# Optimization experiments

Hardware: AMD Instinct MI355X
Metric: run time of the kernel (lower is better)

Reference implementation:

```python
import jax, jax.numpy as jnp
import numpy as np

B, N, D, H, P, S = 2, 40962, 128, 4, 100, 512
HD = D // H  # 32
EPS = 1e-5


def setup_inputs() -> dict:
    key = jax.random.key(0)
    ks = jax.random.split(key, 8)
    s = 1.0 / np.sqrt(D)
    x = jax.random.normal(ks[0], (B, N, D), jnp.float32)
    Wq = jax.random.normal(ks[1], (D, D), jnp.float32) * s
    Wk = jax.random.normal(ks[2], (D, D), jnp.float32) * s
    Wv = jax.random.normal(ks[3], (D, D), jnp.float32) * s
    Wo = jax.random.normal(ks[4], (D, D), jnp.float32) * s
    bq = jnp.zeros((D,), jnp.float32)
    bk = jnp.zeros((D,), jnp.float32)
    bv = jnp.zeros((D,), jnp.float32)
    bo = jnp.zeros((D,), jnp.float32)
    ln_g = jnp.ones((D,), jnp.float32)
    ln_b = jnp.zeros((D,), jnp.float32)
    patch_indices = jax.random.randint(ks[5], (P, S), 0, N)  # node ids per patch slot
    core_mask = jax.random.uniform(ks[6], (P, S)) < 0.8       # core vs overlap slots
    return dict(x=x, Wq=Wq, bq=bq, Wk=Wk, bk=bk, Wv=Wv, bv=bv, Wo=Wo, bo=bo,
                ln_g=ln_g, ln_b=ln_b, patch_indices=patch_indices, core_mask=core_mask)


def reference(x, Wq, bq, Wk, bk, Wv, bv, Wo, bo, ln_g, ln_b, patch_indices, core_mask):
    # gather: [B, P, S, D]
    px = x[:, patch_indices]

    def proj(W, b):
        return (px @ W.T + b).reshape(B, P, S, H, HD)

    q = proj(Wq, bq)
    k = proj(Wk, bk)
    v = proj(Wv, bv)

    # per-patch multi-head attention
    scores = jnp.einsum('bpshd,bpthd->bphst', q, k) / np.sqrt(HD).astype(np.float32)
    attn = jax.nn.softmax(scores, axis=-1)  # dropout is identity in eval
    att = jnp.einsum('bphst,bpthd->bpshd', attn, v).reshape(B, P, S, D)
    patch_out = att @ Wo.T + bo  # [B, P, S, D]

    # scatter-add only core slots back to nodes, with overlap-count normalization
    cm = core_mask.astype(x.dtype)
    patch_out = patch_out * cm[None, :, :, None]
    idx = patch_indices.reshape(-1)  # [P*S]
    vals = patch_out.reshape(B, P * S, D).transpose(1, 0, 2)  # [P*S, B, D]
    agg = jax.ops.segment_sum(vals, idx, num_segments=N).transpose(1, 0, 2)  # [B, N, D]
    cnt = jax.ops.segment_sum(cm.reshape(-1), idx, num_segments=N)  # [N]
    out = agg / jnp.clip(cnt, 1.0)[None, :, None]

    # residual + LayerNorm
    h = x + out
    mu = jnp.mean(h, axis=-1, keepdims=True)
    var = jnp.mean((h - mu) ** 2, axis=-1, keepdims=True)
    return (h - mu) / jnp.sqrt(var + EPS) * ln_g + ln_b
```

## Files before the change

kernel.cpp:

```cpp
#include <hip/hip_runtime.h>
#include <hip/hip_bf16.h>
#include <hip/hip_fp16.h>

#define B_ 2
#define N_ 40962
#define D_ 128
#define H_ 4
#define P_ 100
#define S_ 512
#define T_ 102400
#define PS_ 51200
#define CAP_ 32

typedef unsigned short u16;
typedef unsigned int u32;
typedef _Float16 f16x4 __attribute__((ext_vector_type(4)));
typedef _Float16 f16x8 __attribute__((ext_vector_type(8)));
typedef float f32x4 __attribute__((ext_vector_type(4)));

#define OFF_Q    0ull
#define OFF_K    26214400ull
#define OFF_V    52428800ull
#define OFF_BP   78643200ull
#define OFF_CNT  78774272ull
#define OFF_CM   78938120ull
#define OFF_FLAG 79142920ull
#define CUR_BYTES ((size_t)N_ * 4)

__device__ __forceinline__ u32 pack2h(float a, float b) {
  __half2 h = __floats2half2_rn(a, b);
  return __builtin_bit_cast(u32, h);
}
__device__ __forceinline__ f16x8 cat8(uint2 lo, uint2 hi) {
  return __builtin_bit_cast(f16x8, make_uint4(lo.x, lo.y, hi.x, hi.y));
}

__device__ __forceinline__ f32x4 mfma32(f16x8 a, f16x8 b, f32x4 c) {
#if __has_builtin(__builtin_amdgcn_mfma_f32_16x16x32_f16)
  return __builtin_amdgcn_mfma_f32_16x16x32_f16(a, b, c, 0, 0, 0);
#else
  f16x4 alo = {a[0], a[1], a[2], a[3]}, ahi = {a[4], a[5], a[6], a[7]};
  f16x4 blo = {b[0], b[1], b[2], b[3]}, bhi = {b[4], b[5], b[6], b[7]};
  c = __builtin_amdgcn_mfma_f32_16x16x16f16(alo, blo, c, 0, 0, 0);
  return __builtin_amdgcn_mfma_f32_16x16x16f16(ahi, bhi, c, 0, 0, 0);
#endif
}

__device__ __forceinline__ bool mask_on(const void* mask, int fl, int i) {
  if (fl & 1) return ((const unsigned char*)mask)[i] != 0;
  if (fl & 2) return ((const float*)mask)[i] != 0.f;
  return ((const int*)mask)[i] != 0;
}

__global__ void probe_mask_k(const unsigned char* __restrict__ mb, int* __restrict__ flag) {
  int i = blockIdx.x * 256 + threadIdx.x;
  int f = 0;
  unsigned char v = mb[i];
  if (v) {
    int m4 = i & 3;
    if (m4 == 1) f |= 1;
    else if (m4 == 3) f |= 2;
  }
#pragma unroll
  for (int m = 32; m >= 1; m >>= 1) f |= __shfl_xor(f, m);
  if ((threadIdx.x & 63) == 0 && f) atomicOr(flag, f);
}

__global__ void mask_cnt_k(const void* __restrict__ mask, const int* __restrict__ pidx,
                           const int* __restrict__ flag, float* __restrict__ cm,
                           float* __restrict__ cnt) {
  int i = blockIdx.x * 256 + threadIdx.x;
  int fl = *flag;
  bool on = mask_on(mask, fl, i);
  cm[i] = on ? 1.f : 0.f;
  if (on) atomicAdd(&cnt[pidx[i]], 1.f);
}

__global__ void fill_k(const void* __restrict__ mask, const int* __restrict__ pidx,
                       const int* __restrict__ flag, int* __restrict__ cursor,
                       int* __restrict__ slots) {
  int i = blockIdx.x * 256 + threadIdx.x;
  int fl = *flag;
  if (mask_on(mask, fl, i)) {
    int n = pidx[i];
    int pos = atomicAdd(&cursor[n], 1);
    if (pos < CAP_) slots[n * CAP_ + pos] = i;
  }
}

__global__ void pack_w_k(const float* __restrict__ Wq, const float* __restrict__ Wk,
                         const float* __restrict__ Wv, const float* __restrict__ Wo,
                         u16* __restrict__ bp) {
  int gi = blockIdx.x * 256 + threadIdx.x;
  int m = gi >> 12;
  int r = gi & 4095;
  int fi = r >> 6;
  int l = r & 63;
  int nt = fi >> 3, ks = fi & 7;
  const float* W = (m == 0) ? Wq : (m == 1) ? Wk : (m == 2) ? Wv : Wo;
  int n = nt * 16 + (l & 15);
  int k0 = ks * 16 + ((l >> 4) << 2);
  float4 w = *(const float4*)(W + n * 128 + k0);
  *(uint2*)(bp + (size_t)gi * 4) = make_uint2(pack2h(w.x, w.y), pack2h(w.z, w.w));
}

__global__ __launch_bounds__(256) void qkv_k(
    const float* __restrict__ x, const int* __restrict__ pidx,
    const u16* __restrict__ bp,
    const float* __restrict__ bq, const float* __restrict__ bk, const float* __restrict__ bv,
    u16* __restrict__ qkv) {
  int tid = threadIdx.x;
  int t0 = blockIdx.x * 64;
  int lane = tid & 63, wid = tid >> 6;
  int l15 = lane & 15, l4 = lane >> 4;
  int wm = wid & 1, wn = wid >> 1;
  uint2 afr[2][8];
#pragma unroll
  for (int tt = 0; tt < 2; tt++) {
    int tok = t0 + wm * 32 + tt * 16 + l15;
    int b = (tok >= PS_) ? 1 : 0;
    int ps = tok - b * PS_;
    int pi = pidx[ps];
    const float* rp = x + ((size_t)b * N_ + pi) * D_;
#pragma unroll
    for (int ks = 0; ks < 8; ks++) {
      float4 f = *(const float4*)(rp + ks * 16 + l4 * 4);
      afr[tt][ks] = make_uint2(
          __builtin_bit_cast(u32, __builtin_amdgcn_cvt_pkrtz(f.x, f.y)),
          __builtin_bit_cast(u32, __builtin_amdgcn_cvt_pkrtz(f.z, f.w)));
    }
  }
  const uint2* bpp = (const uint2*)bp;
  u16* qout = qkv;
  u16* kh = qkv + (size_t)T_ * D_;
  u16* vt = qkv + (size_t)2 * T_ * D_;
#pragma unroll 1
  for (int mat = 0; mat < 3; mat++) {
    uint2 bfrag[4][8];
#pragma unroll
    for (int nt = 0; nt < 4; nt++) {
      int ntg = wn * 4 + nt;
#pragma unroll
      for (int ks = 0; ks < 8; ks++)
        bfrag[nt][ks] = bpp[(mat * 64 + ntg * 8 + ks) * 64 + lane];
    }
    if (mat < 2) {
      const float* bias = (mat == 0) ? bq : bk;
      f32x4 acc[4][2];
#pragma unroll
      for (int nt = 0; nt < 4; nt++) {
        float4 b4 = *(const float4*)(bias + wn * 64 + nt * 16 + l4 * 4);
        f32x4 bz = {b4.x, b4.y, b4.z, b4.w};
        acc[nt][0] = bz;
        acc[nt][1] = bz;
      }
#pragma unroll
      for (int kp = 0; kp < 4; kp++) {
#pragma unroll
        for (int nt = 0; nt < 4; nt++) {
          f16x8 a = cat8(bfrag[nt][2 * kp], bfrag[nt][2 * kp + 1]);
#pragma unroll
          for (int tt = 0; tt < 2; tt++) {
            f16x8 b = cat8(afr[tt][2 * kp], afr[tt][2 * kp + 1]);
            acc[nt][tt] = mfma32(a, b, acc[nt][tt]);
          }
        }
      }
#pragma unroll
      for (int tt = 0; tt < 2; tt++) {
        int tok = t0 + wm * 32 + tt * 16 + l15;
#pragma unroll
        for (int nt = 0; nt < 4; nt++) {
          int n0 = wn * 64 + nt * 16 + l4 * 4;
          f32x4 a = acc[nt][tt];
          uint2 pv = make_uint2(pack2h(a[0], a[1]), pack2h(a[2], a[3]));
          if (mat == 0) {
            *(uint2*)(qout + (size_t)tok * D_ + n0) = pv;
          } else {
            int bpi = tok >> 9, s = tok & 511;
            int ch = n0 >> 5, hd = n0 & 31;
            *(uint2*)(kh + ((size_t)(bpi * 4 + ch) * 512 + s) * 32 + hd) = pv;
          }
        }
      }
    } else {
      f32x4 acc[2][4];
#pragma unroll
      for (int nt = 0; nt < 4; nt++) {
        float bvv = bv[wn * 64 + nt * 16 + l15];
#pragma unroll
        for (int mt = 0; mt < 2; mt++) {
          f32x4 z = {bvv, bvv, bvv, bvv};
          acc[mt][nt] = z;
        }
      }
#pragma unroll
      for (int kp = 0; kp < 4; kp++) {
#pragma unroll
        for (int mt = 0; mt < 2; mt++) {
          f16x8 a = cat8(afr[mt][2 * kp], afr[mt][2 * kp + 1]);
#pragma unroll
          for (int nt = 0; nt < 4; nt++) {
            f16x8 b = cat8(bfrag[nt][2 * kp], bfrag[nt][2 * kp + 1]);
            acc[mt][nt] = mfma32(a, b, acc[mt][nt]);
          }
        }
      }
#pragma unroll
      for (int mt = 0; mt < 2; mt++) {
        int rbase = t0 + wm * 32 + mt * 16 + (l4 << 2);
        int bpi = rbase >> 9;
        int s0 = rbase & 511;
#pragma unroll
        for (int nt = 0; nt < 4; nt++) {
          int col = wn * 64 + nt * 16 + l15;
          uint2 pv = make_uint2(pack2h(acc[mt][nt][0], acc[mt][nt][1]),
                                pack2h(acc[mt][nt][2], acc[mt][nt][3]));
          *(uint2*)(vt + ((size_t)(bpi * 4 + (col >> 5)) * 32 + (col & 31)) * 512 + s0) = pv;
        }
      }
    }
  }
}

__global__ __launch_bounds__(512, 4) void attn_k(
    u16* wq_att, const u16* __restrict__ wk, const u16* __restrict__ wvt) {
  __shared__ __align__(16) u16 Ks[512 * 32];
  __shared__ __align__(16) u16 Vs[32 * 512];
  int tid = threadIdx.x;
  int bid = blockIdx.x;
  int h = bid & 3;
  int bp = bid >> 2;
  int lane = tid & 63, w = tid >> 6;
  int l15 = lane & 15, l4 = lane >> 4;
  size_t tbase = (size_t)bp * 512;
  int q0 = w * 64;
  {
    const u16* kg = wk + (size_t)(bp * 4 + h) * 512 * 32;
    const u16* vg = wvt + (size_t)(bp * 4 + h) * 32 * 512;
#pragma unroll
    for (int j = 0; j < 4; j++) {
      int i = j * 512 + tid;
      uint4 ku = *(const uint4*)(kg + (size_t)i * 8);
      int row = i >> 2, c = i & 3;
      int swk = (row >> 1) & 7;
      *(uint2*)(Ks + row * 32 + (((2 * c)     ^ swk) << 2)) = make_uint2(ku.x, ku.y);
      *(uint2*)(Ks + row * 32 + (((2 * c + 1) ^ swk) << 2)) = make_uint2(ku.z, ku.w);
      uint4 vu = *(const uint4*)(vg + (size_t)i * 8);
      int vr2 = i >> 6, vc = i & 63;
      int swv = vr2 & 15;
      *(uint2*)(Vs + vr2 * 512 + (((2 * vc)     ^ swv) << 2)) = make_uint2(vu.x, vu.y);
      *(uint2*)(Vs + vr2 * 512 + (((2 * vc + 1) ^ swv) << 2)) = make_uint2(vu.z, vu.w);
    }
  }
  uint4 qf8[4];
  {
    const u16* qbase = wq_att + (tbase + q0) * 128 + h * 32;
    const __half2 sc2 = __floats2half2_rn(0.25500527f, 0.25500527f);
#pragma unroll
    for (int nt = 0; nt < 4; nt++) {
      const u16* qr = qbase + (size_t)(nt * 16 + l15) * 128 + l4 * 4;
      uint2 u0 = *(const uint2*)(qr);
      uint2 u1 = *(const uint2*)(qr + 16);
      u32 w0 = __builtin_bit_cast(u32, __hmul2(__builtin_bit_cast(__half2, u0.x), sc2));
      u32 w1 = __builtin_bit_cast(u32, __hmul2(__builtin_bit_cast(__half2, u0.y), sc2));
      u32 w2 = __builtin_bit_cast(u32, __hmul2(__builtin_bit_cast(__half2, u1.x), sc2));
      u32 w3 = __builtin_bit_cast(u32, __hmul2(__builtin_bit_cast(__half2, u1.y), sc2));
      qf8[nt] = make_uint4(w0, w1, w2, w3);
    }
  }
  f32x4 O[2][4];
  f32x4 LS[4];
#pragma unroll
  for (int a = 0; a < 4; a++) {
    O[0][a] = (f32x4){0.f, 0.f, 0.f, 0.f};
    O[1][a] = (f32x4){0.f, 0.f, 0.f, 0.f};
    LS[a] = (f32x4){0.f, 0.f, 0.f, 0.f};
  }
  const f16x8 ones8 = {(_Float16)1.f, (_Float16)1.f, (_Float16)1.f, (_Float16)1.f,
                       (_Float16)1.f, (_Float16)1.f, (_Float16)1.f, (_Float16)1.f};
  __syncthreads();

  for (int t0 = 0; t0 < 512; t0 += 64) {
#pragma unroll
    for (int mp = 0; mp < 2; mp++) {
      int krA = t0 + mp * 32 + l15;
      int krB = krA + 16;
      const u16* kpA = Ks + krA * 32;
      const u16* kpB = Ks + krB * 32;
      int swkA = (krA >> 1) & 7;
      int swkB = (krB >> 1) & 7;
      uint2 a0A = *(const uint2*)(kpA + ((l4       ^ swkA) << 2));
      uint2 a1A = *(const uint2*)(kpA + (((4 + l4) ^ swkA) << 2));
      uint2 a0B = *(const uint2*)(kpB + ((l4       ^ swkB) << 2));
      uint2 a1B = *(const uint2*)(kpB + (((4 + l4) ^ swkB) << 2));
      f16x8 a8A = cat8(a0A, a1A);
      f16x8 a8B = cat8(a0B, a1B);
      int gA = (t0 >> 2) + mp * 8 + l4;
      int gB = gA + 4;
      uint2 vA0 = *(const uint2*)(Vs + l15 * 512        + ((gA ^ l15) << 2));
      uint2 vB0 = *(const uint2*)(Vs + l15 * 512        + ((gB ^ l15) << 2));
      uint2 vA1 = *(const uint2*)(Vs + (16 + l15) * 512 + ((gA ^ l15) << 2));
      uint2 vB1 = *(const uint2*)(Vs + (16 + l15) * 512 + ((gB ^ l15) << 2));
      f16x8 v80 = cat8(vA0, vB0);
      f16x8 v81 = cat8(vA1, vB1);
      __builtin_amdgcn_s_setprio(1);
#pragma unroll
      for (int nt = 0; nt < 4; nt++) {
        f16x8 qb = __builtin_bit_cast(f16x8, qf8[nt]);
        f32x4 z = {0.f, 0.f, 0.f, 0.f};
        f32x4 sA = mfma32(a8A, qb, z);
        f32x4 sB = mfma32(a8B, qb, z);
        float e0 = __builtin_amdgcn_exp2f(sA[0]);
        float e1 = __builtin_amdgcn_exp2f(sA[1]);
        float e2 = __builtin_amdgcn_exp2f(sA[2]);
        float e3 = __builtin_amdgcn_exp2f(sA[3]);
        float e4 = __builtin_amdgcn_exp2f(sB[0]);
        float e5 = __builtin_amdgcn_exp2f(sB[1]);
        float e6 = __builtin_amdgcn_exp2f(sB[2]);
        float e7 = __builtin_amdgcn_exp2f(sB[3]);
        uint4 pu = make_uint4(
            __builtin_bit_cast(u32, __builtin_amdgcn_cvt_pkrtz(e0, e1)),
            __builtin_bit_cast(u32, __builtin_amdgcn_cvt_pkrtz(e2, e3)),
            __builtin_bit_cast(u32, __builtin_amdgcn_cvt_pkrtz(e4, e5)),
            __builtin_bit_cast(u32, __builtin_amdgcn_cvt_pkrtz(e6, e7)));
        f16x8 pb = __builtin_bit_cast(f16x8, pu);
        LS[nt]   = mfma32(ones8, pb, LS[nt]);
        O[0][nt] = mfma32(v80, pb, O[0][nt]);
        O[1][nt] = mfma32(v81, pb, O[1][nt]);
      }
      __builtin_amdgcn_s_setprio(0);
    }
  }
#pragma unroll
  for (int nt = 0; nt < 4; nt++) {
    float r = 1.f / LS[nt][0];
#pragma unroll
    for (int mt2 = 0; mt2 < 2; mt2++) {
      uint2 ov = make_uint2(pack2h(O[mt2][nt][0] * r, O[mt2][nt][1] * r),
                            pack2h(O[mt2][nt][2] * r, O[mt2][nt][3] * r));
      *(uint2*)(wq_att + (tbase + q0 + nt * 16 + l15) * 128 + h * 32 + mt2 * 16 + l4 * 4) = ov;
    }
  }
}

__global__ __launch_bounds__(256) void proj_k(
    const u16* __restrict__ watt, const u16* __restrict__ bp, const float* __restrict__ bo,
    u16* __restrict__ po) {
  __shared__ uint4 As[64 * 16];
  int tid = threadIdx.x;
  int t0 = blockIdx.x * 64;
  {
    int r = tid >> 2, qd = tid & 3;
    const uint4* src = (const uint4*)(watt + (size_t)(t0 + r) * D_ + qd * 32);
#pragma unroll
    for (int c = 0; c < 4; c++) {
      int byteoff = (qd * 64 + c * 16) ^ ((r & 7) << 4);
      As[r * 16 + (byteoff >> 4)] = src[c];
    }
  }
  __syncthreads();
  int lane = tid & 63, wid = tid >> 6;
  int l15 = lane & 15, l4 = lane >> 4;
  int wm = wid & 1, wn = wid >> 1;
  uint2 bfrag[4][8];
  const uint2* bpp = (const uint2*)bp;
#pragma unroll
  for (int nt = 0; nt < 4; nt++) {
    int ntg = wn * 4 + nt;
#pragma unroll
    for (int ks = 0; ks < 8; ks++)
      bfrag[nt][ks] = bpp[(3 * 64 + ntg * 8 + ks) * 64 + lane];
  }
  uint2 afr[2][8];
#pragma unroll
  for (int tt = 0; tt < 2; tt++) {
    int row = wm * 32 + tt * 16 + l15;
#pragma unroll
    for (int ks = 0; ks < 8; ks++) {
      int byteoff = (ks * 32 + (l4 << 3)) ^ ((row & 7) << 4);
      afr[tt][ks] = *(const uint2*)((const char*)As + row * 256 + byteoff);
    }
  }
  f32x4 acc[4][2];
#pragma unroll
  for (int nt = 0; nt < 4; nt++) {
    float4 bo4 = *(const float4*)(bo + wn * 64 + nt * 16 + l4 * 4);
    f32x4 bz = {bo4.x, bo4.y, bo4.z, bo4.w};
    acc[nt][0] = bz;
    acc[nt][1] = bz;
  }
#pragma unroll
  for (int kp = 0; kp < 4; kp++) {
#pragma unroll
    for (int nt = 0; nt < 4; nt++) {
      f16x8 a = cat8(bfrag[nt][2 * kp], bfrag[nt][2 * kp + 1]);
#pragma unroll
      for (int tt = 0; tt < 2; tt++) {
        f16x8 b = cat8(afr[tt][2 * kp], afr[tt][2 * kp + 1]);
        acc[nt][tt] = mfma32(a, b, acc[nt][tt]);
      }
    }
  }
#pragma unroll
  for (int tt = 0; tt < 2; tt++) {
    size_t tok = t0 + wm * 32 + tt * 16 + l15;
#pragma unroll
    for (int nt = 0; nt < 4; nt++) {
      int n0 = wn * 64 + nt * 16 + l4 * 4;
      f32x4 a = acc[nt][tt];
      uint2 pv = make_uint2(pack2h(a[0], a[1]), pack2h(a[2], a[3]));
      *(uint2*)(po + tok * D_ + n0) = pv;
    }
  }
}

__global__ __launch_bounds__(256) void ln_k(
    const float* __restrict__ x, const float* __restrict__ cnt,
    const u16* __restrict__ po, const int* __restrict__ slots,
    const float* __restrict__ g, const float* __restrict__ bta, float* __restrict__ out) {
  int tid = threadIdx.x;
  int row = blockIdx.x * 8 + (tid >> 5);
  if (row >= B_ * N_) return;
  int l32 = tid & 31;
  int n = row % N_;
  int b = row / N_;
  float c = cnt[n];
  int deg = (int)c;
  if (deg > CAP_) deg = CAP_;
  float rc = 1.f / (c > 1.f ? c : 1.f);
  float4 a = make_float4(0.f, 0.f, 0.f, 0.f);
  const int* sl = slots + n * CAP_;
  for (int j = 0; j < deg; j++) {
    int s = sl[j];
    uint2 u = *(const uint2*)(po + ((size_t)b * PS_ + s) * D_ + l32 * 4);
    float2 a01 = __half22float2(__builtin_bit_cast(__half2, u.x));
    float2 a23 = __half22float2(__builtin_bit_cast(__half2, u.y));
    a.x += a01.x; a.y += a01.y; a.z += a23.x; a.w += a23.y;
  }
  size_t off = (size_t)row * D_ + l32 * 4;
  float4 xa = *(const float4*)(x + off);
  float4 hv = make_float4(fmaf(a.x, rc, xa.x), fmaf(a.y, rc, xa.y),
                          fmaf(a.z, rc, xa.z), fmaf(a.w, rc, xa.w));
  float s = hv.x + hv.y + hv.z + hv.w;
  float s2 = hv.x * hv.x + hv.y * hv.y + hv.z * hv.z + hv.w * hv.w;
#pragma unroll
  for (int m = 16; m >= 1; m >>= 1) {
    s += __shfl_xor(s, m);
    s2 += __shfl_xor(s2, m);
  }
  float mu = s * 0.0078125f;
  float var = s2 * 0.0078125f - mu * mu;
  float rstd = rsqrtf(var + 1e-5f);
  float4 gv = *(const float4*)(g + l32 * 4);
  float4 bv = *(const float4*)(bta + l32 * 4);
  float4 ov = make_float4((hv.x - mu) * rstd * gv.x + bv.x,
                          (hv.y - mu) * rstd * gv.y + bv.y,
                          (hv.z - mu) * rstd * gv.z + bv.z,
                          (hv.w - mu) * rstd * gv.w + bv.w);
  *(float4*)(out + off) = ov;
}

extern "C" void kernel_launch(void* const* d_in, const int* in_sizes, int n_in,
                              void* d_out, int out_size, void* d_ws, size_t ws_size,
                              hipStream_t stream) {
  const float* x   = (const float*)d_in[0];
  const float* Wq  = (const float*)d_in[1];
  const float* bq  = (const float*)d_in[2];
  const float* Wk  = (const float*)d_in[3];
  const float* bk  = (const float*)d_in[4];
  const float* Wv  = (const float*)d_in[5];
  const float* bv  = (const float*)d_in[6];
  const float* Wo  = (const float*)d_in[7];
  const float* bo  = (const float*)d_in[8];
  const float* lng = (const float*)d_in[9];
  const float* lnb = (const float*)d_in[10];
  const int* pidx  = (const int*)d_in[11];
  const void* cmask = d_in[12];
  float* out = (float*)d_out;
  char* ws = (char*)d_ws;

  u16* wsq = (u16*)(ws + OFF_Q);
  u16* wsk = (u16*)(ws + OFF_K);
  u16* wsvt = (u16*)(ws + OFF_V);
  u16* wbp = (u16*)(ws + OFF_BP);
  float* wcnt = (float*)(ws + OFF_CNT);
  float* wcm  = (float*)(ws + OFF_CM);
  int* wflag  = (int*)(ws + OFF_FLAG);
  u16* po = (u16*)(ws + OFF_K);
  int* cursor = (int*)(ws + OFF_V);
  int* slots = (int*)(ws + OFF_V + CUR_BYTES);

  hipMemsetAsync(ws + OFF_CNT, 0, (OFF_FLAG + 4) - OFF_CNT, stream);

  probe_mask_k<<<200, 256, 0, stream>>>((const unsigned char*)cmask, wflag);
  mask_cnt_k<<<200, 256, 0, stream>>>(cmask, pidx, wflag, wcm, wcnt);
  pack_w_k<<<64, 256, 0, stream>>>(Wq, Wk, Wv, Wo, wbp);
  qkv_k<<<1600, 256, 0, stream>>>(x, pidx, wbp, bq, bk, bv, wsq);
  attn_k<<<800, 512, 0, stream>>>(wsq, wsk, wsvt);
  hipMemsetAsync(cursor, 0, CUR_BYTES, stream);
  fill_k<<<200, 256, 0, stream>>>(cmask, pidx, wflag, cursor, slots);
  proj_k<<<1600, 256, 0, stream>>>(wsq, wbp, bo, po);
  ln_k<<<10241, 256, 0, stream>>>(x, wcnt, po, slots, lng, lnb, out);
}
```

Measured before the change: 163.5 us.

## Stage gathered x rows in swizzled LDS and derive counts from fill cursor

The QKV kernel now gathers each token row cooperatively, with four threads per row reading contiguous 128-byte spans. It converts the values to fp16 and stores them in XOR-swizzled shared memory, from which the MFMA A-fragments are loaded. Previously each lane issued strided float4 reads straight from global memory. Separately, the mask_cnt kernel and its float-atomic count buffer are removed: the layernorm kernel reads the per-node count from the fill cursor, which also shrinks the initial memset. This adds one __syncthreads and 16KB of LDS per block and switches the fp16 conversion from round-toward-zero to round-to-nearest.

```diff
diff --git a/kernel.cpp b/kernel.cpp
--- a/kernel.cpp
+++ b/kernel.cpp
@@ -22,8 +22,6 @@
 #define OFF_K    26214400ull
 #define OFF_V    52428800ull
 #define OFF_BP   78643200ull
-#define OFF_CNT  78774272ull
-#define OFF_CM   78938120ull
 #define OFF_FLAG 79142920ull
 #define CUR_BYTES ((size_t)N_ * 4)
 
@@ -64,16 +62,6 @@
 #pragma unroll
   for (int m = 32; m >= 1; m >>= 1) f |= __shfl_xor(f, m);
   if ((threadIdx.x & 63) == 0 && f) atomicOr(flag, f);
-}
-
-__global__ void mask_cnt_k(const void* __restrict__ mask, const int* __restrict__ pidx,
-                           const int* __restrict__ flag, float* __restrict__ cm,
-                           float* __restrict__ cnt) {
-  int i = blockIdx.x * 256 + threadIdx.x;
-  int fl = *flag;
-  bool on = mask_on(mask, fl, i);
-  cm[i] = on ? 1.f : 0.f;
-  if (on) atomicAdd(&cnt[pidx[i]], 1.f);
 }
 
 __global__ void fill_k(const void* __restrict__ mask, const int* __restrict__ pidx,
@@ -109,25 +97,41 @@
     const u16* __restrict__ bp,
     const float* __restrict__ bq, const float* __restrict__ bk, const float* __restrict__ bv,
     u16* __restrict__ qkv) {
+  __shared__ uint4 As[64 * 16];
   int tid = threadIdx.x;
   int t0 = blockIdx.x * 64;
+  {
+    int r = tid >> 2, qd = tid & 3;
+    int T = t0 + r;
+    int b = T / PS_;
+    int ps = T - b * PS_;
+    int pi = pidx[ps];
+    const float4* src = (const float4*)(x + ((size_t)b * N_ + pi) * D_ + qd * 32);
+    u32 us[16];
+#pragma unroll
+    for (int j = 0; j < 8; j++) {
+      float4 f = src[j];
+      us[2 * j]     = pack2h(f.x, f.y);
+      us[2 * j + 1] = pack2h(f.z, f.w);
+    }
+#pragma unroll
+    for (int c = 0; c < 4; c++) {
+      int byteoff = (qd * 64 + c * 16) ^ ((r & 7) << 4);
+      As[r * 16 + (byteoff >> 4)] = make_uint4(us[4 * c], us[4 * c + 1], us[4 * c + 2], us[4 * c + 3]);
+    }
+  }
+  __syncthreads();
   int lane = tid & 63, wid = tid >> 6;
   int l15 = lane & 15, l4 = lane >> 4;
   int wm = wid & 1, wn = wid >> 1;
   uint2 afr[2][8];
 #pragma unroll
   for (int tt = 0; tt < 2; tt++) {
-    int tok = t0 + wm * 32 + tt * 16 + l15;
-    int b = (tok >= PS_) ? 1 : 0;
-    int ps = tok - b * PS_;
-    int pi = pidx[ps];
-    const float* rp = x + ((size_t)b * N_ + pi) * D_;
+    int row = wm * 32 + tt * 16 + l15;
 #pragma unroll
     for (int ks = 0; ks < 8; ks++) {
-      float4 f = *(const float4*)(rp + ks * 16 + l4 * 4);
-      afr[tt][ks] = make_uint2(
-          __builtin_bit_cast(u32, __builtin_amdgcn_cvt_pkrtz(f.x, f.y)),
-          __builtin_bit_cast(u32, __builtin_amdgcn_cvt_pkrtz(f.z, f.w)));
+      int byteoff = (ks * 32 + (l4 << 3)) ^ ((row & 7) << 4);
+      afr[tt][ks] = *(const uint2*)((const char*)As + row * 256 + byteoff);
     }
   }
   const uint2* bpp = (const uint2*)bp;
@@ -416,7 +420,7 @@
 }
 
 __global__ __launch_bounds__(256) void ln_k(
-    const float* __restrict__ x, const float* __restrict__ cnt,
+    const float* __restrict__ x, const int* __restrict__ cursor,
     const u16* __restrict__ po, const int* __restrict__ slots,
     const float* __restrict__ g, const float* __restrict__ bta, float* __restrict__ out) {
   int tid = threadIdx.x;
@@ -425,10 +429,9 @@
   int l32 = tid & 31;
   int n = row % N_;
   int b = row / N_;
-  float c = cnt[n];
-  int deg = (int)c;
-  if (deg > CAP_) deg = CAP_;
-  float rc = 1.f / (c > 1.f ? c : 1.f);
+  int cnt = cursor[n];
+  int deg = cnt > CAP_ ? CAP_ : cnt;
+  float rc = 1.f / (float)(cnt > 1 ? cnt : 1);
   float4 a = make_float4(0.f, 0.f, 0.f, 0.f);
   const int* sl = slots + n * CAP_;
   for (int j = 0; j < deg; j++) {
@@ -484,22 +487,19 @@
   u16* wsk = (u16*)(ws + OFF_K);
   u16* wsvt = (u16*)(ws + OFF_V);
   u16* wbp = (u16*)(ws + OFF_BP);
-  float* wcnt = (float*)(ws + OFF_CNT);
-  float* wcm  = (float*)(ws + OFF_CM);
   int* wflag  = (int*)(ws + OFF_FLAG);
   u16* po = (u16*)(ws + OFF_K);
   int* cursor = (int*)(ws + OFF_V);
   int* slots = (int*)(ws + OFF_V + CUR_BYTES);
 
-  hipMemsetAsync(ws + OFF_CNT, 0, (OFF_FLAG + 4) - OFF_CNT, stream);
+  hipMemsetAsync(wflag, 0, 4, stream);
 
   probe_mask_k<<<200, 256, 0, stream>>>((const unsigned char*)cmask, wflag);
-  mask_cnt_k<<<200, 256, 0, stream>>>(cmask, pidx, wflag, wcm, wcnt);
   pack_w_k<<<64, 256, 0, stream>>>(Wq, Wk, Wv, Wo, wbp);
   qkv_k<<<1600, 256, 0, stream>>>(x, pidx, wbp, bq, bk, bv, wsq);
   attn_k<<<800, 512, 0, stream>>>(wsq, wsk, wsvt);
   hipMemsetAsync(cursor, 0, CUR_BYTES, stream);
   fill_k<<<200, 256, 0, stream>>>(cmask, pidx, wflag, cursor, slots);
   proj_k<<<1600, 256, 0, stream>>>(wsq, wbp, bo, po);
-  ln_k<<<10241, 256, 0, stream>>>(x, wcnt, po, slots, lng, lnb, out);
-}
+  ln_k<<<10241, 256, 0, stream>>>(x, cursor, po, slots, lng, lnb, out);
+}
```

Result: faster. 154.0 us (-5.8%).
